# Performance work log

Hardware: AMD Instinct MI355X
Metric: run time of the kernel (lower is better)

## Reference

```python
import jax, jax.numpy as jnp
import numpy as np


def setup_inputs() -> dict:
    key = jax.random.key(0)
    k0, k1 = jax.random.split(key)
    b, n, m, e = 8, 2048, 2048, 1024
    mat_0 = jax.random.normal(k0, (b, n, e), dtype=jnp.float32)
    mat_1 = jax.random.normal(k1, (b, m, e), dtype=jnp.float32)
    return {"mat_0": mat_0, "mat_1": mat_1}


def reference(mat_0, mat_1):
    # Original tiles to [b,n,m,e], multiplies, and sums over e.
    # Mathematically identical to a batched QK^T matmul: [b,n,m].
    return jnp.einsum('bne,bme->bnm', mat_0, mat_1)
```

## Files before the change

kernel.cpp:

```cpp
#include <hip/hip_runtime.h>

typedef __attribute__((ext_vector_type(8))) short short8;
typedef __attribute__((ext_vector_type(4))) float f32x4;
typedef __attribute__((ext_vector_type(2))) unsigned int u32x2;
typedef unsigned short u16;

static constexpr int BATCH = 8;
static constexpr int NDIM  = 2048;
static constexpr int MDIM  = 2048;
static constexpr int EDIM  = 1024;
static constexpr int BM    = 256;
static constexpr int BN    = 256;
static constexpr int BK    = 64;

#define BAR() do { asm volatile("" ::: "memory"); \
                   __builtin_amdgcn_s_barrier(); \
                   asm volatile("" ::: "memory"); } while (0)
#define WFENCE() asm volatile("s_waitcnt lgkmcnt(0)" ::: "memory")

__global__ __launch_bounds__(512, 2)
void bmm_fused_kernel(const float* __restrict__ A, const float* __restrict__ B,
                      float* __restrict__ C) {
  __shared__ u16 sh[2][2][BM * BK];

  const int tid  = threadIdx.x;
  const int lane = tid & 63;
  const int wave = tid >> 6;
  const int wr   = wave >> 2;
  const int wc   = wave & 3;
  const int quad = lane >> 4;
  const int ml   = lane & 15;

  const int flat  = (int)blockIdx.x + 8 * (int)blockIdx.y + 64 * (int)blockIdx.z;
  const int nf    = (flat & 7) * 64 + (flat >> 3);
  const int batch = nf >> 6;
  const int trow  = (nf >> 3) & 7;
  const int tcol  = nf & 7;

  const float* Ab = A + (size_t)batch * NDIM * EDIM + (size_t)trow * BM * EDIM;
  const float* Bb = B + (size_t)batch * MDIM * EDIM + (size_t)tcol * BN * EDIM;

  const int rowb = tid >> 4;
  const int colf = (tid & 15) * 4;
  const int swzoff = ((((tid & 15) >> 1) ^ (rowb & 7)) << 3) | ((tid & 1) << 2);
  const float* pA = Ab + (size_t)rowb * EDIM + colf;
  const float* pB = Bb + (size_t)rowb * EDIM + colf;

  const int aBase = (wr * 128 + ml) * 64;
  const int bBase = (wc * 64 + ml) * 64;
  const int kc0 = ((quad    ) ^ (ml & 7)) * 8;
  const int kc1 = ((quad + 4) ^ (ml & 7)) * 8;

  short8 ar[4][2], br[2][2];
  f32x4 acc[8][4] = {};
  f32x4 X[4], Y[4];

#define ISS(Sp, P, h, t) do {                                                  \
    const float* _p = (P) + (size_t)((h) * 128) * EDIM + (size_t)(t) * BK;     \
    Sp[0] = *(const f32x4*)(_p);                                               \
    Sp[1] = *(const f32x4*)(_p + (size_t)32 * EDIM);                           \
    Sp[2] = *(const f32x4*)(_p + (size_t)64 * EDIM);                           \
    Sp[3] = *(const f32x4*)(_p + (size_t)96 * EDIM);                           \
  } while (0)

#define WRT(Sp, buf, ab, h) do {                                               \
    _Pragma("unroll")                                                          \
    for (int _j = 0; _j < 4; ++_j) {                                           \
      unsigned _lo, _hi;                                                       \
      asm("v_cvt_pk_bf16_f32 %0, %1, %2"                                       \
          : "=v"(_lo) : "v"(Sp[_j][0]), "v"(Sp[_j][1]));                       \
      asm("v_cvt_pk_bf16_f32 %0, %1, %2"                                       \
          : "=v"(_hi) : "v"(Sp[_j][2]), "v"(Sp[_j][3]));                       \
      u32x2 _u; _u[0] = _lo; _u[1] = _hi;                                      \
      *(u32x2*)&sh[buf][ab][((h) * 128 + rowb + _j * 32) * 64 + swzoff] = _u;  \
    } } while (0)

#define LDA(buf, mh) do {                                                      \
    _Pragma("unroll")                                                          \
    for (int _q = 0; _q < 4; ++_q) {                                           \
      ar[_q][0] = *(const short8*)&sh[buf][0][aBase + (mh)*4096 + _q*1024 + kc0];\
      ar[_q][1] = *(const short8*)&sh[buf][0][aBase + (mh)*4096 + _q*1024 + kc1];\
    } } while (0)

#define LDB(buf, nh) do {                                                      \
    _Pragma("unroll")                                                          \
    for (int _n = 0; _n < 2; ++_n) {                                           \
      br[_n][0] = *(const short8*)&sh[buf][1][bBase + (nh)*2048 + _n*1024 + kc0];\
      br[_n][1] = *(const short8*)&sh[buf][1][bBase + (nh)*2048 + _n*1024 + kc1];\
    } } while (0)

#define MM(mh, nh) do {                                                        \
    __builtin_amdgcn_s_setprio(1);                                             \
    _Pragma("unroll")                                                          \
    for (int _q = 0; _q < 4; ++_q)                                             \
      _Pragma("unroll")                                                        \
      for (int _n = 0; _n < 2; ++_n)                                           \
        _Pragma("unroll")                                                      \
        for (int _ks = 0; _ks < 2; ++_ks)                                      \
          acc[(mh)*4 + _q][(nh)*2 + _n] = __builtin_amdgcn_mfma_f32_16x16x32_bf16(\
              ar[_q][_ks], br[_n][_ks], acc[(mh)*4 + _q][(nh)*2 + _n], 0, 0, 0);\
    __builtin_amdgcn_s_setprio(0);                                             \
  } while (0)

  ISS(X, pA, 0, 0);
  ISS(Y, pA, 1, 0);
  WRT(X, 0, 0, 0);
  ISS(X, pB, 0, 0);
  WRT(Y, 0, 0, 1);
  ISS(Y, pB, 1, 0);
  WRT(X, 0, 1, 0);
  ISS(X, pA, 0, 1);
  WRT(Y, 0, 1, 1);
  ISS(Y, pA, 1, 1);
  WFENCE();
  BAR();

#pragma unroll 1
  for (int i = 0; i < 7; ++i) {
    const int t1 = 2 * i + 1, p0 = 2 * i + 2, p1 = 2 * i + 3;
    LDA(0, 0); LDB(0, 0);
    WRT(X, 1, 0, 0);
    ISS(X, pB, 0, t1);
    BAR(); MM(0, 0); WFENCE(); BAR();
    LDB(0, 1);
    WRT(Y, 1, 0, 1);
    ISS(Y, pB, 1, t1);
    BAR(); MM(0, 1); WFENCE(); BAR();
    LDA(0, 1);
    WRT(X, 1, 1, 0);
    ISS(X, pA, 0, p0);
    BAR(); MM(1, 1); WFENCE(); BAR();
    LDB(0, 0);
    WRT(Y, 1, 1, 1);
    ISS(Y, pA, 1, p0);
    BAR(); MM(1, 0); WFENCE(); BAR();
    LDA(1, 0); LDB(1, 0);
    WRT(X, 0, 0, 0);
    ISS(X, pB, 0, p0);
    BAR(); MM(0, 0); WFENCE(); BAR();
    LDB(1, 1);
    WRT(Y, 0, 0, 1);
    ISS(Y, pB, 1, p0);
    BAR(); MM(0, 1); WFENCE(); BAR();
    LDA(1, 1);
    WRT(X, 0, 1, 0);
    ISS(X, pA, 0, p1);
    BAR(); MM(1, 1); WFENCE(); BAR();
    LDB(1, 0);
    WRT(Y, 0, 1, 1);
    ISS(Y, pA, 1, p1);
    BAR(); MM(1, 0); WFENCE(); BAR();
  }

  {
    LDA(0, 0); LDB(0, 0);
    WRT(X, 1, 0, 0);
    ISS(X, pB, 0, 15);
    BAR(); MM(0, 0); WFENCE(); BAR();
    LDB(0, 1);
    WRT(Y, 1, 0, 1);
    ISS(Y, pB, 1, 15);
    BAR(); MM(0, 1); WFENCE(); BAR();
    LDA(0, 1);
    WRT(X, 1, 1, 0);
    BAR(); MM(1, 1); WFENCE(); BAR();
    LDB(0, 0);
    WRT(Y, 1, 1, 1);
    BAR(); MM(1, 0); WFENCE(); BAR();
    LDA(1, 0); LDB(1, 0);
    BAR(); MM(0, 0); BAR();
    LDB(1, 1);
    BAR(); MM(0, 1); BAR();
    LDA(1, 1);
    BAR(); MM(1, 1); BAR();
    LDB(1, 0);
    MM(1, 0);
  }

  float* Cb = C + (size_t)batch * NDIM * MDIM
                + (size_t)(trow * BM + wr * 128 + quad * 4) * MDIM
                + (tcol * BN + wc * 64 + ml);
#pragma unroll
  for (int mi = 0; mi < 8; ++mi) {
#pragma unroll
    for (int ni = 0; ni < 4; ++ni) {
      float* cp = Cb + (size_t)(mi * 16) * MDIM + ni * 16;
#pragma unroll
      for (int r = 0; r < 4; ++r)
        cp[(size_t)r * MDIM] = acc[mi][ni][r];
    }
  }
#undef ISS
#undef WRT
#undef LDA
#undef LDB
#undef MM
}

extern "C" void kernel_launch(void* const* d_in, const int* in_sizes, int n_in,
                              void* d_out, int out_size, void* d_ws, size_t ws_size,
                              hipStream_t stream) {
  const float* A = (const float*)d_in[0];
  const float* B = (const float*)d_in[1];
  float*       C = (float*)d_out;
  (void)d_ws; (void)ws_size;

  dim3 grid(MDIM / BN, NDIM / BM, BATCH);
  bmm_fused_kernel<<<grid, dim3(512), 0, stream>>>(A, B, C);
}
```

Measured before the change: 342.7 us.

## Shrink block tile to 128x128 with four waves and drop the epilogue

Halves the block tile from 256x256 to 128x128 and uses 256 threads (four waves, each computing a 64x64 sub-tile), so the grid grows fourfold. The prefetch schedule now uses a single register staging buffer. The separate tail epilogue is replaced by an extra main-loop iteration whose out-of-range prefetch indices are clamped to the last K tile, which adds redundant loads. The goal is more blocks for load balancing and lower per-block register and LDS pressure. The cost is halved operand reuse, which doubles the fp32 global and L2 traffic and the fp32-to-bf16 conversion work per output.

Result: faster. 334.1 us (-2.5%).

```diff
diff --git a/kernel.cpp b/kernel.cpp
--- a/kernel.cpp
+++ b/kernel.cpp
@@ -9,8 +9,8 @@
 static constexpr int NDIM  = 2048;
 static constexpr int MDIM  = 2048;
 static constexpr int EDIM  = 1024;
-static constexpr int BM    = 256;
-static constexpr int BN    = 256;
+static constexpr int BM    = 128;
+static constexpr int BN    = 128;
 static constexpr int BK    = 64;
 
 #define BAR() do { asm volatile("" ::: "memory"); \
@@ -18,7 +18,7 @@
                    asm volatile("" ::: "memory"); } while (0)
 #define WFENCE() asm volatile("s_waitcnt lgkmcnt(0)" ::: "memory")
 
-__global__ __launch_bounds__(512, 2)
+__global__ __launch_bounds__(256, 2)
 void bmm_fused_kernel(const float* __restrict__ A, const float* __restrict__ B,
                       float* __restrict__ C) {
   __shared__ u16 sh[2][2][BM * BK];
@@ -26,162 +26,127 @@
   const int tid  = threadIdx.x;
   const int lane = tid & 63;
   const int wave = tid >> 6;
-  const int wr   = wave >> 2;
-  const int wc   = wave & 3;
   const int quad = lane >> 4;
   const int ml   = lane & 15;
+  const int wrow = (wave >> 1) * 64;
+  const int wcol = (wave & 1) * 64;
 
-  const int flat  = (int)blockIdx.x + 8 * (int)blockIdx.y + 64 * (int)blockIdx.z;
-  const int nf    = (flat & 7) * 64 + (flat >> 3);
-  const int batch = nf >> 6;
-  const int trow  = (nf >> 3) & 7;
-  const int tcol  = nf & 7;
+  const int flat  = (int)blockIdx.x + 16 * (int)blockIdx.y + 256 * (int)blockIdx.z;
+  const int nf    = (flat & 7) * 256 + (flat >> 3);
+  const int batch = nf >> 8;
+  const int trow  = (nf >> 4) & 15;
+  const int tcol  = nf & 15;
 
   const float* Ab = A + (size_t)batch * NDIM * EDIM + (size_t)trow * BM * EDIM;
   const float* Bb = B + (size_t)batch * MDIM * EDIM + (size_t)tcol * BN * EDIM;
 
   const int rowb = tid >> 4;
-  const int colf = (tid & 15) * 4;
-  const int swzoff = ((((tid & 15) >> 1) ^ (rowb & 7)) << 3) | ((tid & 1) << 2);
+  const int ci   = tid & 15;
+  const int colf = ci * 4;
+  const int swzoff = (((ci >> 1) ^ (rowb & 7)) << 3) | ((ci & 1) << 2);
   const float* pA = Ab + (size_t)rowb * EDIM + colf;
   const float* pB = Bb + (size_t)rowb * EDIM + colf;
 
-  const int aBase = (wr * 128 + ml) * 64;
-  const int bBase = (wc * 64 + ml) * 64;
+  const int aOff = (wrow + ml) * 64;
+  const int bOff = (wcol + ml) * 64;
   const int kc0 = ((quad    ) ^ (ml & 7)) * 8;
   const int kc1 = ((quad + 4) ^ (ml & 7)) * 8;
 
-  short8 ar[4][2], br[2][2];
-  f32x4 acc[8][4] = {};
-  f32x4 X[4], Y[4];
+  short8 ar[2][2], br[2][2];
+  f32x4 acc[4][4] = {};
+  f32x4 X[4];
 
-#define ISS(Sp, P, h, t) do {                                                  \
-    const float* _p = (P) + (size_t)((h) * 128) * EDIM + (size_t)(t) * BK;     \
-    Sp[0] = *(const f32x4*)(_p);                                               \
-    Sp[1] = *(const f32x4*)(_p + (size_t)32 * EDIM);                           \
-    Sp[2] = *(const f32x4*)(_p + (size_t)64 * EDIM);                           \
-    Sp[3] = *(const f32x4*)(_p + (size_t)96 * EDIM);                           \
+#define ISS(P, u, t) do {                                                      \
+    const float* _p = (P) + (size_t)((u) * 64) * EDIM + (size_t)(t) * BK;      \
+    X[0] = *(const f32x4*)(_p);                                                \
+    X[1] = *(const f32x4*)(_p + (size_t)16 * EDIM);                            \
+    X[2] = *(const f32x4*)(_p + (size_t)32 * EDIM);                            \
+    X[3] = *(const f32x4*)(_p + (size_t)48 * EDIM);                            \
   } while (0)
 
-#define WRT(Sp, buf, ab, h) do {                                               \
+#define WRT(buf, ab, u) do {                                                   \
     _Pragma("unroll")                                                          \
     for (int _j = 0; _j < 4; ++_j) {                                           \
       unsigned _lo, _hi;                                                       \
       asm("v_cvt_pk_bf16_f32 %0, %1, %2"                                       \
-          : "=v"(_lo) : "v"(Sp[_j][0]), "v"(Sp[_j][1]));                       \
+          : "=v"(_lo) : "v"(X[_j][0]), "v"(X[_j][1]));                         \
       asm("v_cvt_pk_bf16_f32 %0, %1, %2"                                       \
-          : "=v"(_hi) : "v"(Sp[_j][2]), "v"(Sp[_j][3]));                       \
+          : "=v"(_hi) : "v"(X[_j][2]), "v"(X[_j][3]));                         \
       u32x2 _u; _u[0] = _lo; _u[1] = _hi;                                      \
-      *(u32x2*)&sh[buf][ab][((h) * 128 + rowb + _j * 32) * 64 + swzoff] = _u;  \
+      *(u32x2*)&sh[buf][ab][((u) * 64 + rowb + _j * 16) * 64 + swzoff] = _u;   \
     } } while (0)
 
 #define LDA(buf, mh) do {                                                      \
     _Pragma("unroll")                                                          \
-    for (int _q = 0; _q < 4; ++_q) {                                           \
-      ar[_q][0] = *(const short8*)&sh[buf][0][aBase + (mh)*4096 + _q*1024 + kc0];\
-      ar[_q][1] = *(const short8*)&sh[buf][0][aBase + (mh)*4096 + _q*1024 + kc1];\
+    for (int _s = 0; _s < 2; ++_s) {                                           \
+      ar[_s][0] = *(const short8*)&sh[buf][0][aOff + ((mh)*32 + _s*16)*64 + kc0];\
+      ar[_s][1] = *(const short8*)&sh[buf][0][aOff + ((mh)*32 + _s*16)*64 + kc1];\
     } } while (0)
 
 #define LDB(buf, nh) do {                                                      \
     _Pragma("unroll")                                                          \
-    for (int _n = 0; _n < 2; ++_n) {                                           \
-      br[_n][0] = *(const short8*)&sh[buf][1][bBase + (nh)*2048 + _n*1024 + kc0];\
-      br[_n][1] = *(const short8*)&sh[buf][1][bBase + (nh)*2048 + _n*1024 + kc1];\
+    for (int _s = 0; _s < 2; ++_s) {                                           \
+      br[_s][0] = *(const short8*)&sh[buf][1][bOff + ((nh)*32 + _s*16)*64 + kc0];\
+      br[_s][1] = *(const short8*)&sh[buf][1][bOff + ((nh)*32 + _s*16)*64 + kc1];\
     } } while (0)
 
 #define MM(mh, nh) do {                                                        \
     __builtin_amdgcn_s_setprio(1);                                             \
     _Pragma("unroll")                                                          \
-    for (int _q = 0; _q < 4; ++_q)                                             \
+    for (int _sa = 0; _sa < 2; ++_sa)                                          \
       _Pragma("unroll")                                                        \
-      for (int _n = 0; _n < 2; ++_n)                                           \
+      for (int _sb = 0; _sb < 2; ++_sb)                                        \
         _Pragma("unroll")                                                      \
         for (int _ks = 0; _ks < 2; ++_ks)                                      \
-          acc[(mh)*4 + _q][(nh)*2 + _n] = __builtin_amdgcn_mfma_f32_16x16x32_bf16(\
-              ar[_q][_ks], br[_n][_ks], acc[(mh)*4 + _q][(nh)*2 + _n], 0, 0, 0);\
+          acc[(mh)*2 + _sa][(nh)*2 + _sb] = __builtin_amdgcn_mfma_f32_16x16x32_bf16(\
+              ar[_sa][_ks], br[_sb][_ks], acc[(mh)*2 + _sa][(nh)*2 + _sb], 0, 0, 0);\
     __builtin_amdgcn_s_setprio(0);                                             \
   } while (0)
 
-  ISS(X, pA, 0, 0);
-  ISS(Y, pA, 1, 0);
-  WRT(X, 0, 0, 0);
-  ISS(X, pB, 0, 0);
-  WRT(Y, 0, 0, 1);
-  ISS(Y, pB, 1, 0);
-  WRT(X, 0, 1, 0);
-  ISS(X, pA, 0, 1);
-  WRT(Y, 0, 1, 1);
-  ISS(Y, pA, 1, 1);
+  ISS(pA, 0, 0); WRT(0, 0, 0);
+  ISS(pA, 1, 0); WRT(0, 0, 1);
+  ISS(pB, 0, 0); WRT(0, 1, 0);
+  ISS(pB, 1, 0); WRT(0, 1, 1);
+  ISS(pA, 0, 1);
   WFENCE();
   BAR();
 
 #pragma unroll 1
-  for (int i = 0; i < 7; ++i) {
-    const int t1 = 2 * i + 1, p0 = 2 * i + 2, p1 = 2 * i + 3;
+  for (int i = 0; i < 8; ++i) {
+    const int t1  = 2 * i + 1;
+    const int tp0 = (2 * i + 2 < 15) ? 2 * i + 2 : 15;
+    const int tp1 = (2 * i + 3 < 15) ? 2 * i + 3 : 15;
     LDA(0, 0); LDB(0, 0);
-    WRT(X, 1, 0, 0);
-    ISS(X, pB, 0, t1);
+    WRT(1, 0, 0); ISS(pA, 1, t1);
     BAR(); MM(0, 0); WFENCE(); BAR();
     LDB(0, 1);
-    WRT(Y, 1, 0, 1);
-    ISS(Y, pB, 1, t1);
+    WRT(1, 0, 1); ISS(pB, 0, t1);
     BAR(); MM(0, 1); WFENCE(); BAR();
     LDA(0, 1);
-    WRT(X, 1, 1, 0);
-    ISS(X, pA, 0, p0);
+    WRT(1, 1, 0); ISS(pB, 1, t1);
     BAR(); MM(1, 1); WFENCE(); BAR();
     LDB(0, 0);
-    WRT(Y, 1, 1, 1);
-    ISS(Y, pA, 1, p0);
+    WRT(1, 1, 1); ISS(pA, 0, tp0);
     BAR(); MM(1, 0); WFENCE(); BAR();
     LDA(1, 0); LDB(1, 0);
-    WRT(X, 0, 0, 0);
-    ISS(X, pB, 0, p0);
+    WRT(0, 0, 0); ISS(pA, 1, tp0);
     BAR(); MM(0, 0); WFENCE(); BAR();
     LDB(1, 1);
-    WRT(Y, 0, 0, 1);
-    ISS(Y, pB, 1, p0);
+    WRT(0, 0, 1); ISS(pB, 0, tp0);
     BAR(); MM(0, 1); WFENCE(); BAR();
     LDA(1, 1);
-    WRT(X, 0, 1, 0);
-    ISS(X, pA, 0, p1);
+    WRT(0, 1, 0); ISS(pB, 1, tp0);
     BAR(); MM(1, 1); WFENCE(); BAR();
     LDB(1, 0);
-    WRT(Y, 0, 1, 1);
-    ISS(Y, pA, 1, p1);
+    WRT(0, 1, 1); ISS(pA, 0, tp1);
     BAR(); MM(1, 0); WFENCE(); BAR();
   }
 
-  {
-    LDA(0, 0); LDB(0, 0);
-    WRT(X, 1, 0, 0);
-    ISS(X, pB, 0, 15);
-    BAR(); MM(0, 0); WFENCE(); BAR();
-    LDB(0, 1);
-    WRT(Y, 1, 0, 1);
-    ISS(Y, pB, 1, 15);
-    BAR(); MM(0, 1); WFENCE(); BAR();
-    LDA(0, 1);
-    WRT(X, 1, 1, 0);
-    BAR(); MM(1, 1); WFENCE(); BAR();
-    LDB(0, 0);
-    WRT(Y, 1, 1, 1);
-    BAR(); MM(1, 0); WFENCE(); BAR();
-    LDA(1, 0); LDB(1, 0);
-    BAR(); MM(0, 0); BAR();
-    LDB(1, 1);
-    BAR(); MM(0, 1); BAR();
-    LDA(1, 1);
-    BAR(); MM(1, 1); BAR();
-    LDB(1, 0);
-    MM(1, 0);
-  }
-
   float* Cb = C + (size_t)batch * NDIM * MDIM
-                + (size_t)(trow * BM + wr * 128 + quad * 4) * MDIM
-                + (tcol * BN + wc * 64 + ml);
+                + (size_t)(trow * BM + wrow + quad * 4) * MDIM
+                + (tcol * BN + wcol + ml);
 #pragma unroll
-  for (int mi = 0; mi < 8; ++mi) {
+  for (int mi = 0; mi < 4; ++mi) {
 #pragma unroll
     for (int ni = 0; ni < 4; ++ni) {
       float* cp = Cb + (size_t)(mi * 16) * MDIM + ni * 16;
@@ -206,5 +171,5 @@
   (void)d_ws; (void)ws_size;
 
   dim3 grid(MDIM / BN, NDIM / BM, BATCH);
-  bmm_fused_kernel<<<grid, dim3(512), 0, stream>>>(A, B, C);
+  bmm_fused_kernel<<<grid, dim3(256), 0, stream>>>(A, B, C);
 }
```
